# Performance work log

Hardware: AMD Instinct MI355X
Metric: run time of the kernel (lower is better)

Reference implementation:

```python
import jax, jax.numpy as jnp
import numpy as np

B, S, D_IN, D_OUT = 4, 2048, 1024, 1024


def setup_inputs() -> dict:
    key = jax.random.key(0)
    k1, k2, k3, k4 = jax.random.split(key, 4)
    x = jax.random.normal(k1, (B, S, D_IN), dtype=jnp.float32)
    # torch nn.Linear weight layout: [d_out, d_in]
    wq = jax.random.normal(k2, (D_OUT, D_IN), dtype=jnp.float32) * (1.0 / np.sqrt(D_IN))
    wk = jax.random.normal(k3, (D_OUT, D_IN), dtype=jnp.float32) * (1.0 / np.sqrt(D_IN))
    wv = jax.random.normal(k4, (D_OUT, D_IN), dtype=jnp.float32) * (1.0 / np.sqrt(D_IN))
    return {"x": x, "wq": wq, "wk": wk, "wv": wv}


def reference(x, wq, wk, wv):
    # q,k,v: [b, s, d_out]
    q = jnp.einsum('bsd,od->bso', x, wq)
    k = jnp.einsum('bsd,od->bso', x, wk)
    v = jnp.einsum('bsd,od->bso', x, wv)
    scale = 1.0 / jnp.sqrt(jnp.asarray(k.shape[-1], dtype=q.dtype))
    scores = jnp.einsum('bqd,bkd->bqk', q, k)  # [b, s, s]
    s = scores.shape[-1]
    causal = jnp.tril(jnp.ones((s, s), dtype=bool))
    scores = jnp.where(causal, scores, -jnp.inf)
    attn = jax.nn.softmax(scores * scale, axis=-1)
    # dropout p=0.0 -> identity
    return jnp.einsum('bqk,bkd->bqd', attn, v)
```

## Files before the change

### kernel.cpp

```cpp
#include <hip/hip_runtime.h>
#include <hip/hip_bf16.h>
#include <cstdint>

#define BATCH 4
#define SEQ   2048
#define DIN   1024
#define DOUT  1024
#define SCALE 0.03125f

typedef unsigned short u16;
typedef float  f32x4  __attribute__((ext_vector_type(4)));
typedef __bf16 bf16x8 __attribute__((ext_vector_type(8)));

__device__ __forceinline__ u16 f2bf(float f) {
    unsigned u = __float_as_uint(f);
    unsigned r = 0x7fffu + ((u >> 16) & 1u);
    return (u16)((u + r) >> 16);
}

__device__ __forceinline__ f32x4 mfma16(bf16x8 a, bf16x8 b, f32x4 c) {
    return __builtin_amdgcn_mfma_f32_16x16x32_bf16(a, b, c, 0, 0, 0);
}

__device__ __forceinline__ void gl_lds16(const u16* g, u16* l) {
    __builtin_amdgcn_global_load_lds(
        (const __attribute__((address_space(1))) unsigned int*)g,
        (__attribute__((address_space(3))) unsigned int*)l, 16, 0, 0);
}

#define BAR    asm volatile("s_barrier" ::: "memory")
#define VMCNT4 asm volatile("s_waitcnt vmcnt(4)" ::: "memory")
#define VMCNT6 asm volatile("s_waitcnt vmcnt(6)" ::: "memory")
#define VMCNT0 asm volatile("s_waitcnt vmcnt(0)" ::: "memory")
#define LGKM0  asm volatile("s_waitcnt lgkmcnt(0)" ::: "memory")

__global__ __launch_bounds__(256) void cvt_all(const float* __restrict__ x,
                                               const float* __restrict__ wq,
                                               const float* __restrict__ wk,
                                               const float* __restrict__ wv,
                                               u16* __restrict__ dst) {
    const size_t NX = (size_t)BATCH * SEQ * DIN;
    size_t e = ((size_t)blockIdx.x * 256 + threadIdx.x) * 8;
    const float* src;
    size_t off;
    if (e < NX) { src = x; off = e; }
    else {
        size_t r = e - NX;
        int w = (int)(r >> 20);
        src = (w == 0) ? wq : (w == 1) ? wk : wv;
        off = r & ((1u << 20) - 1);
    }
    f32x4 a = *(const f32x4*)(src + off);
    f32x4 b = *(const f32x4*)(src + off + 4);
    uint4 o;
    o.x = (unsigned)f2bf(a[0]) | ((unsigned)f2bf(a[1]) << 16);
    o.y = (unsigned)f2bf(a[2]) | ((unsigned)f2bf(a[3]) << 16);
    o.z = (unsigned)f2bf(b[0]) | ((unsigned)f2bf(b[1]) << 16);
    o.w = (unsigned)f2bf(b[2]) | ((unsigned)f2bf(b[3]) << 16);
    *(uint4*)(dst + e) = o;
}

__device__ __forceinline__ void stg128(const u16* __restrict__ g, int ld,
                                       u16* unit, int tid) {
#pragma unroll
    for (int i = 0; i < 2; i++) {
        int D = (i * 512 + tid) * 16;
        int r = D >> 7, w = D & 127;
        int gcol = (w ^ ((r & 7) << 4)) >> 1;
        gl_lds16(g + (size_t)r * ld + gcol, unit + (i * 512 + (tid >> 6) * 64) * 8);
    }
}

__device__ __forceinline__ void rd4(const u16* unit, int rowbase, int l15, int l4,
                                    bf16x8 f[4][2]) {
    const char* u = (const char*)unit;
#pragma unroll
    for (int i = 0; i < 4; i++) {
        int row = rowbase + i * 16 + l15;
#pragma unroll
        for (int kk = 0; kk < 2; kk++)
            f[i][kk] = *(const bf16x8*)(u + row * 128 +
                                        ((kk * 64 + l4 * 16) ^ ((row & 7) << 4)));
    }
}

__device__ __forceinline__ void rd2(const u16* unit, int rowbase, int l15, int l4,
                                    bf16x8 f[2][2]) {
    const char* u = (const char*)unit;
#pragma unroll
    for (int i = 0; i < 2; i++) {
        int row = rowbase + i * 16 + l15;
#pragma unroll
        for (int kk = 0; kk < 2; kk++)
            f[i][kk] = *(const bf16x8*)(u + row * 128 +
                                        ((kk * 64 + l4 * 16) ^ ((row & 7) << 4)));
    }
}

#define G128_PH1(AC, BC)                                                         \
    rd4((AC), wm * 64, l15, l4, a);                                              \
    rd2((BC) + (wn >> 1) * 8192, browb, l15, l4, b01);                           \
    rd2((BC) + (wn >> 1) * 8192, browb + 32, l15, l4, b23);                      \
    BAR;                                                                         \
    __builtin_amdgcn_s_setprio(1);                                               \
    _Pragma("unroll") for (int kk = 0; kk < 2; kk++)                             \
    _Pragma("unroll") for (int mi = 0; mi < 4; mi++)                             \
    _Pragma("unroll") for (int j = 0; j < 2; j++)                                \
        acc[mi][j] = mfma16(b01[j][kk], a[mi][kk], acc[mi][j]);                  \
    __builtin_amdgcn_s_setprio(0);                                               \
    LGKM0;                                                                       \
    BAR;

#define G128_PH2(CURB, K2)                                                       \
    stg128(Ag_ + (K2), LDA_, lds + (CURB), tid);                                 \
    stg128(Bg_ + (K2), LDB_, lds + (CURB) + 8192, tid);                          \
    stg128(Bg_ + (size_t)128 * LDB_ + (K2), LDB_, lds + (CURB) + 16384, tid);    \
    VMCNT6; BAR;                                                                 \
    __builtin_amdgcn_s_setprio(1);                                               \
    _Pragma("unroll") for (int kk = 0; kk < 2; kk++)                             \
    _Pragma("unroll") for (int mi = 0; mi < 4; mi++)                             \
    _Pragma("unroll") for (int j = 0; j < 2; j++)                                \
        acc[mi][2 + j] = mfma16(b23[j][kk], a[mi][kk], acc[mi][2 + j]);          \
    __builtin_amdgcn_s_setprio(0);                                               \
    BAR;

#define G128_BODY(Ag, LDA, Bg, LDB, NKT)                                         \
    f32x4 acc[4][4] = {};                                                        \
    bf16x8 a[4][2], b01[2][2], b23[2][2];                                        \
    const u16* Ag_ = (Ag); const u16* Bg_ = (Bg);                                \
    const int LDA_ = (LDA), LDB_ = (LDB), NKT_ = (NKT);                          \
    const int browb = (wn & 1) * 64;                                             \
    stg128(Ag_, LDA_, lds, tid);                                                 \
    stg128(Bg_, LDB_, lds + 8192, tid);                                          \
    stg128(Bg_ + (size_t)128 * LDB_, LDB_, lds + 16384, tid);                    \
    stg128(Ag_ + 64, LDA_, lds + 24576, tid);                                    \
    stg128(Bg_ + 64, LDB_, lds + 24576 + 8192, tid);                             \
    stg128(Bg_ + (size_t)128 * LDB_ + 64, LDB_, lds + 24576 + 16384, tid);       \
    VMCNT6; BAR;                                                                 \
    for (int t = 0; t < NKT_; t += 2) {                                          \
        {                                                                        \
            const int k2 = ((t + 2 < NKT_) ? t + 2 : NKT_ - 1) * 64;             \
            G128_PH1(lds, lds + 8192)                                            \
            G128_PH2(0, k2)                                                      \
        }                                                                        \
        {                                                                        \
            const int k2 = ((t + 3 < NKT_) ? t + 3 : NKT_ - 1) * 64;             \
            G128_PH1(lds + 24576, lds + 24576 + 8192)                            \
            G128_PH2(24576, k2)                                                  \
        }                                                                        \
    }                                                                            \
    VMCNT0;

__device__ __forceinline__ void stg_half(const u16* __restrict__ gbase,
                                         u16* unit, int tid) {
#pragma unroll
    for (int i = 0; i < 2; i++) {
        int D = (i * 512 + tid) * 16;
        int r = D >> 7, w = D & 127;
        int gcol = (w ^ ((r & 7) << 4)) >> 1;
        gl_lds16(gbase + (size_t)r * DIN + gcol,
                 unit + (i * 512 + (tid >> 6) * 64) * 8);
    }
}

__device__ __forceinline__ void rdA8(const u16* unit, int mh, int l15, int l4,
                                     int sw, bf16x8 a[4][2]) {
    const char* u = (const char*)unit;
#pragma unroll
    for (int mi = 0; mi < 4; mi++)
#pragma unroll
        for (int kk = 0; kk < 2; kk++)
            a[mi][kk] = *(const bf16x8*)(u + (mh * 64 + mi * 16 + l15) * 128 +
                                         ((kk * 64 + l4 * 16) ^ sw));
}

__device__ __forceinline__ void rdB8(const u16* unit, int wn1, int nh, int l15,
                                     int l4, int sw, bf16x8 b[2][2]) {
    const char* u = (const char*)unit;
#pragma unroll
    for (int ni = 0; ni < 2; ni++)
#pragma unroll
        for (int kk = 0; kk < 2; kk++)
            b[ni][kk] = *(const bf16x8*)(u + (wn1 * 64 + nh * 32 + ni * 16 + l15) * 128 +
                                         ((kk * 64 + l4 * 16) ^ sw));
}

#define QUAD(MH, NH)                                                         \
    __builtin_amdgcn_s_setprio(1);                                           \
    _Pragma("unroll") for (int kk = 0; kk < 2; kk++)                         \
    _Pragma("unroll") for (int mi = 0; mi < 4; mi++)                         \
    _Pragma("unroll") for (int ni = 0; ni < 2; ni++)                         \
        acc[(MH)*4 + mi][(NH)*2 + ni] =                                      \
            mfma16(bb[NH][ni][kk], a[mi][kk], acc[(MH)*4 + mi][(NH)*2 + ni]);\
    __builtin_amdgcn_s_setprio(0);

__global__ __launch_bounds__(512) void qkv_gemm256(const u16* __restrict__ xb,
                                                   const u16* __restrict__ wb,
                                                   u16* __restrict__ qkv) {
    extern __shared__ __align__(16) u16 lds[];
    const int tid = threadIdx.x, lane = tid & 63, wid = tid >> 6;
    const int wm = wid >> 2, wn = wid & 3, bh = wn >> 1, wn1 = wn & 1;
    const int l15 = lane & 15, l4 = lane >> 4;
    const int sw = (l15 & 7) << 4;

    u16* A00 = lds;              u16* A01 = lds + 8192;
    u16* A10 = lds + 16384;      u16* A11 = lds + 24576;
    u16* B00 = lds + 32768;      u16* B01 = lds + 40960;
    u16* B10 = lds + 49152;      u16* B11 = lds + 57344;
    u16* Ar0 = lds + wm * 8192;
    u16* Ar1 = lds + 16384 + wm * 8192;
    u16* Br0 = lds + 32768 + bh * 8192;
    u16* Br1 = lds + 49152 + bh * 8192;

    for (int tile = blockIdx.x; tile < 384; tile += 256) {
        const int xcd = tile & 7, li = tile >> 3;
        const int mt = xcd * 4 + li / 12, nt = li % 12;
        const int m0 = mt * 256, n0 = nt * 256;
        const u16* Ag = xb + (size_t)m0 * DIN;
        const u16* Bg = wb + (size_t)n0 * DIN;
        f32x4 acc[8][4] = {};
        bf16x8 a[4][2], bb[2][2][2];

        stg_half(Bg,                          B00, tid);
        stg_half(Bg + (size_t)128 * DIN,      B01, tid);
        stg_half(Ag,                          A00, tid);
        stg_half(Ag + (size_t)128 * DIN,      A01, tid);
        stg_half(Bg + 64,                     B10, tid);
        stg_half(Bg + (size_t)128 * DIN + 64, B11, tid);
        VMCNT4; BAR;

        for (int i = 0; i < 8; i++) {
            const int t1k = (2 * i + 1) * 64;
            const int k2 = ((2 * i + 2 < 16) ? 2 * i + 2 : 15) * 64;
            const int k3 = ((2 * i + 3 < 16) ? 2 * i + 3 : 15) * 64;
            rdA8(Ar0, 0, l15, l4, sw, a);
            rdB8(Br0, wn1, 0, l15, l4, sw, bb[0]);
            stg_half(Ag + t1k, A10, tid);
            BAR; QUAD(0, 0); BAR;
            rdB8(Br0, wn1, 1, l15, l4, sw, bb[1]);
            stg_half(Ag + (size_t)128 * DIN + t1k, A11, tid);
            BAR; QUAD(0, 1); BAR;
            rdA8(Ar0, 1, l15, l4, sw, a);
            stg_half(Bg + k2, B00, tid);
            BAR; QUAD(1, 0); BAR;
            stg_half(Bg + (size_t)128 * DIN + k2, B01, tid);
            VMCNT4; BAR; QUAD(1, 1); BAR;
            rdA8(Ar1, 0, l15, l4, sw, a);
            rdB8(Br1, wn1, 0, l15, l4, sw, bb[0]);
            stg_half(Ag + k2, A00, tid);
            BAR; QUAD(0, 0); BAR;
            rdB8(Br1, wn1, 1, l15, l4, sw, bb[1]);
            stg_half(Ag + (size_t)128 * DIN + k2, A01, tid);
            BAR; QUAD(0, 1); BAR;
            rdA8(Ar1, 1, l15, l4, sw, a);
            stg_half(Bg + k3, B10, tid);
            BAR; QUAD(1, 0); BAR;
            stg_half(Bg + (size_t)128 * DIN + k3, B11, tid);
            VMCNT4; BAR; QUAD(1, 1); BAR;
        }
        VMCNT0;

        const int wsel = n0 >> 10, c0 = n0 & 1023;
        u16* Op = qkv + (size_t)wsel * ((size_t)BATCH * SEQ * DOUT);
#pragma unroll
        for (int ai = 0; ai < 8; ai++) {
            int row = m0 + wm * 128 + ai * 16 + l15;
#pragma unroll
            for (int bj = 0; bj < 4; bj++) {
                int col = c0 + wn * 64 + bj * 16 + l4 * 4;
                uint2 o;
                o.x = (unsigned)f2bf(acc[ai][bj][0]) | ((unsigned)f2bf(acc[ai][bj][1]) << 16);
                o.y = (unsigned)f2bf(acc[ai][bj][2]) | ((unsigned)f2bf(acc[ai][bj][3]) << 16);
                *(uint2*)&Op[(size_t)row * DOUT + col] = o;
            }
        }
    }
}

__global__ __launch_bounds__(256) void vtrans(const u16* __restrict__ v,
                                              u16* __restrict__ vt) {
    __shared__ __align__(16) u16 t[64][80];
    const int s0 = blockIdx.x * 64, d0 = blockIdx.y * 64;
    const size_t bo = (size_t)blockIdx.z * SEQ * DOUT;
    const int tid = threadIdx.x;
#pragma unroll
    for (int i = 0; i < 2; i++) {
        int e = (tid + i * 256) * 8;
        int r = e >> 6, c = e & 63;
        *(uint4*)&t[r][c] = *(const uint4*)&v[bo + (size_t)(s0 + r) * DOUT + d0 + c];
    }
    __syncthreads();
#pragma unroll
    for (int i = 0; i < 2; i++) {
        int e = (tid + i * 256) * 8;
        int rd = e >> 6, cs = e & 63;
        u16 tmp[8];
#pragma unroll
        for (int j = 0; j < 8; j++) tmp[j] = t[cs + j][rd];
        uint4 o;
        o.x = (unsigned)tmp[0] | ((unsigned)tmp[1] << 16);
        o.y = (unsigned)tmp[2] | ((unsigned)tmp[3] << 16);
        o.z = (unsigned)tmp[4] | ((unsigned)tmp[5] << 16);
        o.w = (unsigned)tmp[6] | ((unsigned)tmp[7] << 16);
        *(uint4*)&vt[(size_t)blockIdx.z * DOUT * SEQ + (size_t)(d0 + rd) * SEQ + s0 + cs] = o;
    }
}

__global__ __launch_bounds__(512) void qk3(const u16* __restrict__ qg,
                                           const u16* __restrict__ kg,
                                           u16* __restrict__ sg) {
    extern __shared__ __align__(16) u16 lds[];
    const int bxx = blockIdx.x, batch = blockIdx.y;
    int mt = 0, base = 0;
#pragma unroll 16
    for (int m = 0; m < 16; m++) {
        int c = (m >> 1) + 1;
        if (bxx < base + c) { mt = m; break; }
        base += c;
    }
    const int nt = bxx - base;
    const int m0 = mt * 128, n0 = nt * 256;
    const int tid = threadIdx.x, lane = tid & 63;
    const int wm = (tid >> 6) >> 2, wn = (tid >> 6) & 3;
    const int l15 = lane & 15, l4 = lane >> 4;
    const size_t bo = (size_t)batch * SEQ * DOUT;
    const u16* Aq = qg + bo + (size_t)m0 * DOUT;
    const u16* Bk = kg + bo + (size_t)n0 * DOUT;

    G128_BODY(Aq, DOUT, Bk, DOUT, 16)

    u16* Sp = sg + (size_t)batch * SEQ * SEQ;
#pragma unroll
    for (int ai = 0; ai < 4; ai++) {
        int q = m0 + wm * 64 + ai * 16 + l15;
#pragma unroll
        for (int bj = 0; bj < 4; bj++) {
            int kc = n0 + wn * 64 + bj * 16 + l4 * 4;
            u16 v0 = (kc + 0 <= q) ? f2bf(acc[ai][bj][0] * SCALE) : (u16)0xFF80;
            u16 v1 = (kc + 1 <= q) ? f2bf(acc[ai][bj][1] * SCALE) : (u16)0xFF80;
            u16 v2 = (kc + 2 <= q) ? f2bf(acc[ai][bj][2] * SCALE) : (u16)0xFF80;
            u16 v3 = (kc + 3 <= q) ? f2bf(acc[ai][bj][3] * SCALE) : (u16)0xFF80;
            uint2 o;
            o.x = (unsigned)v0 | ((unsigned)v1 << 16);
            o.y = (unsigned)v2 | ((unsigned)v3 << 16);
            *(uint2*)&Sp[(size_t)q * SEQ + kc] = o;
        }
    }
}

__global__ __launch_bounds__(512) void pv3(const u16* __restrict__ pg,
                                           const u16* __restrict__ vtg,
                                           float* __restrict__ og) {
    extern __shared__ __align__(16) u16 lds[];
    const int mt = blockIdx.x, batch = blockIdx.z;
    const int m0 = mt * 128, n0 = blockIdx.y * 256;
    const int nkt = (mt + 1) * 2;
    const int tid = threadIdx.x, lane = tid & 63;
    const int wm = (tid >> 6) >> 2, wn = (tid >> 6) & 3;
    const int l15 = lane & 15, l4 = lane >> 4;
    const u16* Ap = pg + (size_t)batch * SEQ * SEQ + (size_t)m0 * SEQ;
    const u16* Bv = vtg + (size_t)batch * DOUT * SEQ + (size_t)n0 * SEQ;

    G128_BODY(Ap, SEQ, Bv, SEQ, nkt)

    float* Oq = og + (size_t)batch * SEQ * DOUT;
#pragma unroll
    for (int ai = 0; ai < 4; ai++) {
        int q = m0 + wm * 64 + ai * 16 + l15;
#pragma unroll
        for (int bj = 0; bj < 4; bj++) {
            int d = n0 + wn * 64 + bj * 16 + l4 * 4;
            *(f32x4*)&Oq[(size_t)q * DOUT + d] = acc[ai][bj];
        }
    }
}

__global__ __launch_bounds__(256) void softmax_rows(u16* __restrict__ sg) {
    const int row = blockIdx.x * 4 + (threadIdx.x >> 6);
    const int lane = threadIdx.x & 63;
    const int b = row >> 11, q = row & 2047;
    u16* srow = sg + (size_t)b * SEQ * SEQ + (size_t)q * SEQ;
    const int kend = ((q >> 7) + 1) << 7;
    float v[4][8];
    float m = -__builtin_inff();
#pragma unroll
    for (int c = 0; c < 4; c++) {
        int k = c * 512 + lane * 8;
        if (k < kend) {
            uint4 x = *(const uint4*)&srow[k];
            unsigned w0 = x.x, w1 = x.y, w2 = x.z, w3 = x.w;
            v[c][0] = __uint_as_float(w0 << 16); v[c][1] = __uint_as_float(w0 & 0xffff0000u);
            v[c][2] = __uint_as_float(w1 << 16); v[c][3] = __uint_as_float(w1 & 0xffff0000u);
            v[c][4] = __uint_as_float(w2 << 16); v[c][5] = __uint_as_float(w2 & 0xffff0000u);
            v[c][6] = __uint_as_float(w3 << 16); v[c][7] = __uint_as_float(w3 & 0xffff0000u);
        } else {
#pragma unroll
            for (int j = 0; j < 8; j++) v[c][j] = -__builtin_inff();
        }
#pragma unroll
        for (int j = 0; j < 8; j++) m = fmaxf(m, v[c][j]);
    }
#pragma unroll
    for (int off = 32; off >= 1; off >>= 1) m = fmaxf(m, __shfl_xor(m, off));
    float s = 0.f;
#pragma unroll
    for (int c = 0; c < 4; c++)
#pragma unroll
        for (int j = 0; j < 8; j++) { v[c][j] = __expf(v[c][j] - m); s += v[c][j]; }
#pragma unroll
    for (int off = 32; off >= 1; off >>= 1) s += __shfl_xor(s, off);
    float inv = 1.f / s;
#pragma unroll
    for (int c = 0; c < 4; c++) {
        int k = c * 512 + lane * 8;
        if (k < kend) {
            uint4 o;
            o.x = (unsigned)f2bf(v[c][0] * inv) | ((unsigned)f2bf(v[c][1] * inv) << 16);
            o.y = (unsigned)f2bf(v[c][2] * inv) | ((unsigned)f2bf(v[c][3] * inv) << 16);
            o.z = (unsigned)f2bf(v[c][4] * inv) | ((unsigned)f2bf(v[c][5] * inv) << 16);
            o.w = (unsigned)f2bf(v[c][6] * inv) | ((unsigned)f2bf(v[c][7] * inv) << 16);
            *(uint4*)&srow[k] = o;
        }
    }
}

extern "C" void kernel_launch(void* const* d_in, const int* in_sizes, int n_in,
                              void* d_out, int out_size, void* d_ws, size_t ws_size,
                              hipStream_t stream) {
    const float* x  = (const float*)d_in[0];
    const float* wq = (const float*)d_in[1];
    const float* wk = (const float*)d_in[2];
    const float* wv = (const float*)d_in[3];
    float* out = (float*)d_out;

    const size_t NX  = (size_t)BATCH * SEQ * DIN;
    const size_t NWT = (size_t)DOUT * DIN;
    u16* xb  = (u16*)d_ws;
    u16* wb  = xb + NX;
    u16* qkv = wb + 3 * NWT;
    u16* vt  = qkv + 3 * NX;
    u16* sb  = vt + NX;

    cvt_all<<<(NX + 3 * NWT) / 8 / 256, 256, 0, stream>>>(x, wq, wk, wv, xb);

    (void)hipFuncSetAttribute((const void*)qkv_gemm256,
                              hipFuncAttributeMaxDynamicSharedMemorySize, 131072);
    (void)hipFuncSetAttribute((const void*)qk3,
                              hipFuncAttributeMaxDynamicSharedMemorySize, 98304);
    (void)hipFuncSetAttribute((const void*)pv3,
                              hipFuncAttributeMaxDynamicSharedMemorySize, 98304);

    qkv_gemm256<<<dim3(256), dim3(512), 131072, stream>>>(xb, wb, qkv);

    vtrans<<<dim3(SEQ / 64, DOUT / 64, BATCH), 256, 0, stream>>>(qkv + 2 * NX, vt);

    qk3<<<dim3(72, BATCH), dim3(512), 98304, stream>>>(qkv, qkv + NX, sb);

    softmax_rows<<<(BATCH * SEQ) / 4, 256, 0, stream>>>(sb);

    pv3<<<dim3(16, 4, 4), dim3(512), 98304, stream>>>(sb, vt, out);
}
```

Baseline: 183.3 us.

## Fuse V transpose into QKV GEMM epilogue and retile QK/PV to 128x128

The QKV projection epilogue now writes the V tile transposed through LDS straight into the vt buffer, which removes the separate vtrans kernel and its extra pass over V. The QK and PV GEMMs change from 128x256 to 128x128 tiles with a new 64-LDS-KB body, giving more blocks and less LDS per block. PV pairs a short causal row tile with a long one (pr and 15-pr) to balance work across blocks. The tile-to-XCD mapping in the QKV GEMM is also reordered. Stores of Q, K, S and O become per-element scalar writes with swapped MFMA operand order, which may hurt store coalescing.

```diff
diff --git a/kernel.cpp b/kernel.cpp
--- a/kernel.cpp
+++ b/kernel.cpp
@@ -30,7 +30,6 @@
 
 #define BAR    asm volatile("s_barrier" ::: "memory")
 #define VMCNT4 asm volatile("s_waitcnt vmcnt(4)" ::: "memory")
-#define VMCNT6 asm volatile("s_waitcnt vmcnt(6)" ::: "memory")
 #define VMCNT0 asm volatile("s_waitcnt vmcnt(0)" ::: "memory")
 #define LGKM0  asm volatile("s_waitcnt lgkmcnt(0)" ::: "memory")
 
@@ -84,72 +83,83 @@
     }
 }
 
-__device__ __forceinline__ void rd2(const u16* unit, int rowbase, int l15, int l4,
-                                    bf16x8 f[2][2]) {
+__device__ __forceinline__ void rd2k(const u16* unit, int row0, int l15, int l4,
+                                     bf16x8 f[2]) {
     const char* u = (const char*)unit;
-#pragma unroll
-    for (int i = 0; i < 2; i++) {
-        int row = rowbase + i * 16 + l15;
-#pragma unroll
-        for (int kk = 0; kk < 2; kk++)
-            f[i][kk] = *(const bf16x8*)(u + row * 128 +
-                                        ((kk * 64 + l4 * 16) ^ ((row & 7) << 4)));
-    }
-}
-
-#define G128_PH1(AC, BC)                                                         \
-    rd4((AC), wm * 64, l15, l4, a);                                              \
-    rd2((BC) + (wn >> 1) * 8192, browb, l15, l4, b01);                           \
-    rd2((BC) + (wn >> 1) * 8192, browb + 32, l15, l4, b23);                      \
-    BAR;                                                                         \
-    __builtin_amdgcn_s_setprio(1);                                               \
-    _Pragma("unroll") for (int kk = 0; kk < 2; kk++)                             \
-    _Pragma("unroll") for (int mi = 0; mi < 4; mi++)                             \
-    _Pragma("unroll") for (int j = 0; j < 2; j++)                                \
-        acc[mi][j] = mfma16(b01[j][kk], a[mi][kk], acc[mi][j]);                  \
-    __builtin_amdgcn_s_setprio(0);                                               \
-    LGKM0;                                                                       \
-    BAR;
-
-#define G128_PH2(CURB, K2)                                                       \
-    stg128(Ag_ + (K2), LDA_, lds + (CURB), tid);                                 \
-    stg128(Bg_ + (K2), LDB_, lds + (CURB) + 8192, tid);                          \
-    stg128(Bg_ + (size_t)128 * LDB_ + (K2), LDB_, lds + (CURB) + 16384, tid);    \
-    VMCNT6; BAR;                                                                 \
-    __builtin_amdgcn_s_setprio(1);                                               \
-    _Pragma("unroll") for (int kk = 0; kk < 2; kk++)                             \
-    _Pragma("unroll") for (int mi = 0; mi < 4; mi++)                             \
-    _Pragma("unroll") for (int j = 0; j < 2; j++)                                \
-        acc[mi][2 + j] = mfma16(b23[j][kk], a[mi][kk], acc[mi][2 + j]);          \
-    __builtin_amdgcn_s_setprio(0);                                               \
-    BAR;
-
-#define G128_BODY(Ag, LDA, Bg, LDB, NKT)                                         \
-    f32x4 acc[4][4] = {};                                                        \
-    bf16x8 a[4][2], b01[2][2], b23[2][2];                                        \
-    const u16* Ag_ = (Ag); const u16* Bg_ = (Bg);                                \
-    const int LDA_ = (LDA), LDB_ = (LDB), NKT_ = (NKT);                          \
-    const int browb = (wn & 1) * 64;                                             \
-    stg128(Ag_, LDA_, lds, tid);                                                 \
-    stg128(Bg_, LDB_, lds + 8192, tid);                                          \
-    stg128(Bg_ + (size_t)128 * LDB_, LDB_, lds + 16384, tid);                    \
-    stg128(Ag_ + 64, LDA_, lds + 24576, tid);                                    \
-    stg128(Bg_ + 64, LDB_, lds + 24576 + 8192, tid);                             \
-    stg128(Bg_ + (size_t)128 * LDB_ + 64, LDB_, lds + 24576 + 16384, tid);       \
-    VMCNT6; BAR;                                                                 \
-    for (int t = 0; t < NKT_; t += 2) {                                          \
-        {                                                                        \
-            const int k2 = ((t + 2 < NKT_) ? t + 2 : NKT_ - 1) * 64;             \
-            G128_PH1(lds, lds + 8192)                                            \
-            G128_PH2(0, k2)                                                      \
-        }                                                                        \
-        {                                                                        \
-            const int k2 = ((t + 3 < NKT_) ? t + 3 : NKT_ - 1) * 64;             \
-            G128_PH1(lds + 24576, lds + 24576 + 8192)                            \
-            G128_PH2(24576, k2)                                                  \
-        }                                                                        \
-    }                                                                            \
+    int row = row0 + l15;
+#pragma unroll
+    for (int kk = 0; kk < 2; kk++)
+        f[kk] = *(const bf16x8*)(u + row * 128 +
+                                 ((kk * 64 + l4 * 16) ^ ((row & 7) << 4)));
+}
+
+__device__ __forceinline__ void g64_body(u16* lds, const u16* __restrict__ Ag,
+                                         int lda, const u16* __restrict__ Bg,
+                                         int ldb, int nkt, int wm, int wn,
+                                         int l15, int l4, int tid,
+                                         f32x4 acc[4][2]) {
+    bf16x8 a[4][2], b0[2], b1[2];
+    u16* A0 = lds;          u16* B0 = lds + 8192;
+    u16* A1 = lds + 16384;  u16* B1 = lds + 24576;
+    stg128(Ag, lda, A0, tid);      stg128(Bg, ldb, B0, tid);
+    stg128(Ag + 64, lda, A1, tid); stg128(Bg + 64, ldb, B1, tid);
+    VMCNT4; BAR;
+    for (int t = 0; t < nkt; t += 2) {
+        {
+            const int k2 = ((t + 2 < nkt) ? t + 2 : nkt - 1) * 64;
+            rd4(A0, wm * 64, l15, l4, a);
+            rd2k(B0, wn * 32, l15, l4, b0);
+            rd2k(B0, wn * 32 + 16, l15, l4, b1);
+            BAR;
+            __builtin_amdgcn_s_setprio(1);
+#pragma unroll
+            for (int kk = 0; kk < 2; kk++)
+#pragma unroll
+                for (int mi = 0; mi < 4; mi++)
+                    acc[mi][0] = mfma16(a[mi][kk], b0[kk], acc[mi][0]);
+            __builtin_amdgcn_s_setprio(0);
+            LGKM0; BAR;
+            stg128(Ag + k2, lda, A0, tid);
+            stg128(Bg + k2, ldb, B0, tid);
+            VMCNT4; BAR;
+            __builtin_amdgcn_s_setprio(1);
+#pragma unroll
+            for (int kk = 0; kk < 2; kk++)
+#pragma unroll
+                for (int mi = 0; mi < 4; mi++)
+                    acc[mi][1] = mfma16(a[mi][kk], b1[kk], acc[mi][1]);
+            __builtin_amdgcn_s_setprio(0);
+            BAR;
+        }
+        {
+            const int k3 = ((t + 3 < nkt) ? t + 3 : nkt - 1) * 64;
+            rd4(A1, wm * 64, l15, l4, a);
+            rd2k(B1, wn * 32, l15, l4, b0);
+            rd2k(B1, wn * 32 + 16, l15, l4, b1);
+            BAR;
+            __builtin_amdgcn_s_setprio(1);
+#pragma unroll
+            for (int kk = 0; kk < 2; kk++)
+#pragma unroll
+                for (int mi = 0; mi < 4; mi++)
+                    acc[mi][0] = mfma16(a[mi][kk], b0[kk], acc[mi][0]);
+            __builtin_amdgcn_s_setprio(0);
+            LGKM0; BAR;
+            stg128(Ag + k3, lda, A1, tid);
+            stg128(Bg + k3, ldb, B1, tid);
+            VMCNT4; BAR;
+            __builtin_amdgcn_s_setprio(1);
+#pragma unroll
+            for (int kk = 0; kk < 2; kk++)
+#pragma unroll
+                for (int mi = 0; mi < 4; mi++)
+                    acc[mi][1] = mfma16(a[mi][kk], b1[kk], acc[mi][1]);
+            __builtin_amdgcn_s_setprio(0);
+            BAR;
+        }
+    }
     VMCNT0;
+}
 
 __device__ __forceinline__ void stg_half(const u16* __restrict__ gbase,
                                          u16* unit, int tid) {
@@ -191,12 +201,13 @@
     _Pragma("unroll") for (int mi = 0; mi < 4; mi++)                         \
     _Pragma("unroll") for (int ni = 0; ni < 2; ni++)                         \
         acc[(MH)*4 + mi][(NH)*2 + ni] =                                      \
-            mfma16(bb[NH][ni][kk], a[mi][kk], acc[(MH)*4 + mi][(NH)*2 + ni]);\
+            mfma16(a[mi][kk], bb[NH][ni][kk], acc[(MH)*4 + mi][(NH)*2 + ni]);\
     __builtin_amdgcn_s_setprio(0);
 
 __global__ __launch_bounds__(512) void qkv_gemm256(const u16* __restrict__ xb,
                                                    const u16* __restrict__ wb,
-                                                   u16* __restrict__ qkv) {
+                                                   u16* __restrict__ qkv,
+                                                   u16* __restrict__ vt) {
     extern __shared__ __align__(16) u16 lds[];
     const int tid = threadIdx.x, lane = tid & 63, wid = tid >> 6;
     const int wm = wid >> 2, wn = wid & 3, bh = wn >> 1, wn1 = wn & 1;
@@ -213,8 +224,8 @@
     u16* Br1 = lds + 49152 + bh * 8192;
 
     for (int tile = blockIdx.x; tile < 384; tile += 256) {
-        const int xcd = tile & 7, li = tile >> 3;
-        const int mt = xcd * 4 + li / 12, nt = li % 12;
+        const int wg = (tile & 7) * 48 + (tile >> 3);
+        const int mt = wg & 31, nt = wg >> 5;
         const int m0 = mt * 256, n0 = nt * 256;
         const u16* Ag = xb + (size_t)m0 * DIN;
         const u16* Bg = wb + (size_t)n0 * DIN;
@@ -261,117 +272,118 @@
         VMCNT0;
 
         const int wsel = n0 >> 10, c0 = n0 & 1023;
-        u16* Op = qkv + (size_t)wsel * ((size_t)BATCH * SEQ * DOUT);
-#pragma unroll
-        for (int ai = 0; ai < 8; ai++) {
-            int row = m0 + wm * 128 + ai * 16 + l15;
-#pragma unroll
-            for (int bj = 0; bj < 4; bj++) {
-                int col = c0 + wn * 64 + bj * 16 + l4 * 4;
-                uint2 o;
-                o.x = (unsigned)f2bf(acc[ai][bj][0]) | ((unsigned)f2bf(acc[ai][bj][1]) << 16);
-                o.y = (unsigned)f2bf(acc[ai][bj][2]) | ((unsigned)f2bf(acc[ai][bj][3]) << 16);
-                *(uint2*)&Op[(size_t)row * DOUT + col] = o;
+        if (wsel < 2) {
+            u16* Op = qkv + (size_t)wsel * ((size_t)BATCH * SEQ * DOUT);
+#pragma unroll
+            for (int ai = 0; ai < 8; ai++)
+#pragma unroll
+                for (int bj = 0; bj < 4; bj++)
+#pragma unroll
+                    for (int rr = 0; rr < 4; rr++) {
+                        int row = m0 + wm * 128 + ai * 16 + l4 * 4 + rr;
+                        int col = c0 + wn * 64 + bj * 16 + l15;
+                        Op[(size_t)row * DOUT + col] = f2bf(acc[ai][bj][rr]);
+                    }
+        } else {
+            BAR;
+#pragma unroll
+            for (int ai = 0; ai < 8; ai++)
+#pragma unroll
+                for (int bj = 0; bj < 4; bj++) {
+                    int dloc = wn * 64 + bj * 16 + l15;
+                    int sloc = wm * 128 + ai * 16 + l4 * 4;
+                    int byte = (dloc * 512 + sloc * 2) ^ ((dloc & 7) << 4);
+                    uint2 o;
+                    o.x = (unsigned)f2bf(acc[ai][bj][0]) |
+                          ((unsigned)f2bf(acc[ai][bj][1]) << 16);
+                    o.y = (unsigned)f2bf(acc[ai][bj][2]) |
+                          ((unsigned)f2bf(acc[ai][bj][3]) << 16);
+                    *(uint2*)((char*)lds + byte) = o;
+                }
+            BAR;
+            const int batch = m0 >> 11, s0 = m0 & 2047;
+            u16* Vt = vt + (size_t)batch * DOUT * SEQ;
+#pragma unroll
+            for (int i = 0; i < 16; i++) {
+                int e = (i * 512 + tid) * 16;
+                int dloc = e >> 9, sb = e & 511;
+                int byte = e ^ ((dloc & 7) << 4);
+                uint4 v = *(const uint4*)((char*)lds + byte);
+                *(uint4*)&Vt[(size_t)(c0 + dloc) * SEQ + s0 + (sb >> 1)] = v;
             }
-        }
-    }
-}
-
-__global__ __launch_bounds__(256) void vtrans(const u16* __restrict__ v,
-                                              u16* __restrict__ vt) {
-    __shared__ __align__(16) u16 t[64][80];
-    const int s0 = blockIdx.x * 64, d0 = blockIdx.y * 64;
-    const size_t bo = (size_t)blockIdx.z * SEQ * DOUT;
-    const int tid = threadIdx.x;
-#pragma unroll
-    for (int i = 0; i < 2; i++) {
-        int e = (tid + i * 256) * 8;
-        int r = e >> 6, c = e & 63;
-        *(uint4*)&t[r][c] = *(const uint4*)&v[bo + (size_t)(s0 + r) * DOUT + d0 + c];
-    }
-    __syncthreads();
-#pragma unroll
-    for (int i = 0; i < 2; i++) {
-        int e = (tid + i * 256) * 8;
-        int rd = e >> 6, cs = e & 63;
-        u16 tmp[8];
-#pragma unroll
-        for (int j = 0; j < 8; j++) tmp[j] = t[cs + j][rd];
-        uint4 o;
-        o.x = (unsigned)tmp[0] | ((unsigned)tmp[1] << 16);
-        o.y = (unsigned)tmp[2] | ((unsigned)tmp[3] << 16);
-        o.z = (unsigned)tmp[4] | ((unsigned)tmp[5] << 16);
-        o.w = (unsigned)tmp[6] | ((unsigned)tmp[7] << 16);
-        *(uint4*)&vt[(size_t)blockIdx.z * DOUT * SEQ + (size_t)(d0 + rd) * SEQ + s0 + cs] = o;
-    }
-}
-
-__global__ __launch_bounds__(512) void qk3(const u16* __restrict__ qg,
-                                           const u16* __restrict__ kg,
-                                           u16* __restrict__ sg) {
+            LGKM0; BAR;
+        }
+    }
+}
+
+__global__ __launch_bounds__(512) void qk_g64(const u16* __restrict__ qg,
+                                              const u16* __restrict__ kg,
+                                              u16* __restrict__ sg) {
     extern __shared__ __align__(16) u16 lds[];
     const int bxx = blockIdx.x, batch = blockIdx.y;
     int mt = 0, base = 0;
 #pragma unroll 16
     for (int m = 0; m < 16; m++) {
-        int c = (m >> 1) + 1;
+        int c = m + 1;
         if (bxx < base + c) { mt = m; break; }
         base += c;
     }
     const int nt = bxx - base;
-    const int m0 = mt * 128, n0 = nt * 256;
+    const int m0 = mt * 128, n0 = nt * 128;
     const int tid = threadIdx.x, lane = tid & 63;
     const int wm = (tid >> 6) >> 2, wn = (tid >> 6) & 3;
     const int l15 = lane & 15, l4 = lane >> 4;
     const size_t bo = (size_t)batch * SEQ * DOUT;
-    const u16* Aq = qg + bo + (size_t)m0 * DOUT;
-    const u16* Bk = kg + bo + (size_t)n0 * DOUT;
-
-    G128_BODY(Aq, DOUT, Bk, DOUT, 16)
+
+    f32x4 acc[4][2] = {};
+    g64_body(lds, qg + bo + (size_t)m0 * DOUT, DOUT,
+             kg + bo + (size_t)n0 * DOUT, DOUT, 16,
+             wm, wn, l15, l4, tid, acc);
 
     u16* Sp = sg + (size_t)batch * SEQ * SEQ;
 #pragma unroll
-    for (int ai = 0; ai < 4; ai++) {
-        int q = m0 + wm * 64 + ai * 16 + l15;
-#pragma unroll
-        for (int bj = 0; bj < 4; bj++) {
-            int kc = n0 + wn * 64 + bj * 16 + l4 * 4;
-            u16 v0 = (kc + 0 <= q) ? f2bf(acc[ai][bj][0] * SCALE) : (u16)0xFF80;
-            u16 v1 = (kc + 1 <= q) ? f2bf(acc[ai][bj][1] * SCALE) : (u16)0xFF80;
-            u16 v2 = (kc + 2 <= q) ? f2bf(acc[ai][bj][2] * SCALE) : (u16)0xFF80;
-            u16 v3 = (kc + 3 <= q) ? f2bf(acc[ai][bj][3] * SCALE) : (u16)0xFF80;
-            uint2 o;
-            o.x = (unsigned)v0 | ((unsigned)v1 << 16);
-            o.y = (unsigned)v2 | ((unsigned)v3 << 16);
-            *(uint2*)&Sp[(size_t)q * SEQ + kc] = o;
-        }
-    }
-}
-
-__global__ __launch_bounds__(512) void pv3(const u16* __restrict__ pg,
-                                           const u16* __restrict__ vtg,
-                                           float* __restrict__ og) {
+    for (int ai = 0; ai < 4; ai++)
+#pragma unroll
+        for (int bj = 0; bj < 2; bj++)
+#pragma unroll
+            for (int rr = 0; rr < 4; rr++) {
+                int q = m0 + wm * 64 + ai * 16 + l4 * 4 + rr;
+                int kc = n0 + wn * 32 + bj * 16 + l15;
+                Sp[(size_t)q * SEQ + kc] =
+                    (kc <= q) ? f2bf(acc[ai][bj][rr] * SCALE) : (u16)0xFF80;
+            }
+}
+
+__global__ __launch_bounds__(512) void pv_g64(const u16* __restrict__ pg,
+                                              const u16* __restrict__ vtg,
+                                              float* __restrict__ og) {
     extern __shared__ __align__(16) u16 lds[];
-    const int mt = blockIdx.x, batch = blockIdx.z;
-    const int m0 = mt * 128, n0 = blockIdx.y * 256;
-    const int nkt = (mt + 1) * 2;
+    const int pr = blockIdx.x;
+    const int n0 = blockIdx.y * 128, batch = blockIdx.z;
     const int tid = threadIdx.x, lane = tid & 63;
     const int wm = (tid >> 6) >> 2, wn = (tid >> 6) & 3;
     const int l15 = lane & 15, l4 = lane >> 4;
-    const u16* Ap = pg + (size_t)batch * SEQ * SEQ + (size_t)m0 * SEQ;
-    const u16* Bv = vtg + (size_t)batch * DOUT * SEQ + (size_t)n0 * SEQ;
-
-    G128_BODY(Ap, SEQ, Bv, SEQ, nkt)
-
-    float* Oq = og + (size_t)batch * SEQ * DOUT;
-#pragma unroll
-    for (int ai = 0; ai < 4; ai++) {
-        int q = m0 + wm * 64 + ai * 16 + l15;
-#pragma unroll
-        for (int bj = 0; bj < 4; bj++) {
-            int d = n0 + wn * 64 + bj * 16 + l4 * 4;
-            *(f32x4*)&Oq[(size_t)q * DOUT + d] = acc[ai][bj];
-        }
+    const u16* Pb = pg + (size_t)batch * SEQ * SEQ;
+    const u16* Vb = vtg + (size_t)batch * DOUT * SEQ + (size_t)n0 * SEQ;
+    float* Ob = og + (size_t)batch * SEQ * DOUT;
+
+#pragma unroll
+    for (int half = 0; half < 2; half++) {
+        const int mt = half ? (15 - pr) : pr;
+        const int m0 = mt * 128;
+        f32x4 acc[4][2] = {};
+        g64_body(lds, Pb + (size_t)m0 * SEQ, SEQ, Vb, SEQ, (mt + 1) * 2,
+                 wm, wn, l15, l4, tid, acc);
+#pragma unroll
+        for (int ai = 0; ai < 4; ai++)
+#pragma unroll
+            for (int bj = 0; bj < 2; bj++)
+#pragma unroll
+                for (int rr = 0; rr < 4; rr++) {
+                    int q = m0 + wm * 64 + ai * 16 + l4 * 4 + rr;
+                    int d = n0 + wn * 32 + bj * 16 + l15;
+                    Ob[(size_t)q * DOUT + d] = acc[ai][bj][rr];
+                }
     }
 }
 
@@ -445,18 +457,16 @@
 
     (void)hipFuncSetAttribute((const void*)qkv_gemm256,
                               hipFuncAttributeMaxDynamicSharedMemorySize, 131072);
-    (void)hipFuncSetAttribute((const void*)qk3,
-                              hipFuncAttributeMaxDynamicSharedMemorySize, 98304);
-    (void)hipFuncSetAttribute((const void*)pv3,
-                              hipFuncAttributeMaxDynamicSharedMemorySize, 98304);
-
-    qkv_gemm256<<<dim3(256), dim3(512), 131072, stream>>>(xb, wb, qkv);
-
-    vtrans<<<dim3(SEQ / 64, DOUT / 64, BATCH), 256, 0, stream>>>(qkv + 2 * NX, vt);
-
-    qk3<<<dim3(72, BATCH), dim3(512), 98304, stream>>>(qkv, qkv + NX, sb);
+    (void)hipFuncSetAttribute((const void*)qk_g64,
+                              hipFuncAttributeMaxDynamicSharedMemorySize, 65536);
+    (void)hipFuncSetAttribute((const void*)pv_g64,
+                              hipFuncAttributeMaxDynamicSharedMemorySize, 65536);
+
+    qkv_gemm256<<<dim3(256), dim3(512), 131072, stream>>>(xb, wb, qkv, vt);
+
+    qk_g64<<<dim3(136, BATCH), dim3(512), 65536, stream>>>(qkv, qkv + NX, sb);
 
     softmax_rows<<<(BATCH * SEQ) / 4, 256, 0, stream>>>(sb);
 
-    pv3<<<dim3(16, 4, 4), dim3(512), 98304, stream>>>(sb, vt, out);
-}
+    pv_g64<<<dim3(8, 8, 4), dim3(512), 65536, stream>>>(sb, vt, out);
+}
```

Measured after the change: 184.8 us. About the same (+0.8%).
